# Kernel tuning notes

Measured on AMD Instinct MI355X. Metric: run time of the kernel, lower is better.

The kernel has to match this reference:

```python
import jax, jax.numpy as jnp
import numpy as np


def _l2norm(t, eps=1e-12):
    # matches torch F.normalize(p=2, dim=-1): x / max(||x||_2, eps)
    n = jnp.sqrt(jnp.sum(t * t, axis=-1, keepdims=True))
    return t / jnp.maximum(n, eps)


def setup_inputs() -> dict:
    key = jax.random.key(0)
    ks = jax.random.split(key, 8)
    B, N, C, H, W = 16, 4, 256, 64, 64
    d = 64  # dim_head
    x = jax.random.normal(ks[0], (B, C, H, W), jnp.float32)
    fmaps = jax.random.normal(ks[1], (B, N, C, H, W), jnp.float32)
    Wq = jax.random.normal(ks[2], (N * d, C), jnp.float32) * 0.02   # Linear [out,in]
    Wk = jax.random.normal(ks[3], (N, d, C), jnp.float32) * 0.02    # grouped 1x1 conv, per-group [d,C]
    Wv = jax.random.normal(ks[4], (N, d, C), jnp.float32) * 0.02
    rescale = jnp.ones((N, 1, 1), jnp.float32)
    Wffn = jax.random.normal(ks[5], (C, N * d), jnp.float32) * 0.02
    bffn = jnp.zeros((C,), jnp.float32)
    return {"x": x, "fmaps": fmaps, "Wq": Wq, "Wk": Wk, "Wv": Wv,
            "rescale": rescale, "Wffn": Wffn, "bffn": bffn}


def reference(x, fmaps, Wq, Wk, Wv, rescale, Wffn, bffn):
    B, N, C, H, W = fmaps.shape
    d = Wk.shape[1]
    HW = H * W

    # x: [B,C,H,W] -> tokens [B,HW,C]
    x_in = jnp.transpose(x, (0, 2, 3, 1)).reshape(B, HW, C)
    q_in = jnp.einsum('bsc,oc->bso', x_in, Wq)            # [B,HW,N*d]

    # grouped 1x1 convs on fmaps (group = fmap index n)
    fm = fmaps.reshape(B, N, C, HW)                       # [B,N,C,HW]
    k = jnp.einsum('bncs,ndc->bnds', fm, Wk)              # [B,N,d,HW]
    v = jnp.einsum('bncs,ndc->bnds', fm, Wv)              # [B,N,d,HW]

    q = jnp.transpose(q_in.reshape(B, HW, N, d), (0, 2, 3, 1))  # [B,N,d,HW]

    qn = _l2norm(q)   # normalize over spatial (HW) axis
    kn = _l2norm(k)

    attn = jnp.einsum('bnds,bnes->bnde', kn, qn) * rescale      # [B,N,d,d]
    attn = jax.nn.softmax(attn, axis=-1)
    out = jnp.einsum('bnde,bnes->bnds', attn, v)                # [B,N,d,HW]

    out = jnp.transpose(out, (0, 3, 1, 2)).reshape(B, HW, N * d)  # [B,HW,N*d]
    out = out + q_in
    out = jnp.einsum('bsi,ci->bsc', out, Wffn) + bffn + q_in      # ffn + residual
    return jnp.transpose(out.reshape(B, H, W, C), (0, 3, 1, 2))   # [B,C,H,W]
```

## Files before the change

### kernel.cpp

```cpp
#include <hip/hip_runtime.h>
#include <hip/hip_bf16.h>
#include <cmath>

using bf16 = __hip_bfloat16;
typedef __attribute__((ext_vector_type(4))) float  f32x4;
typedef __attribute__((ext_vector_type(8))) short  bf16x8;
typedef unsigned int u32;
typedef unsigned short u16;

__device__ __forceinline__ void gl_lds16(const bf16* g, bf16* l) {
    __builtin_amdgcn_global_load_lds(
        (const __attribute__((address_space(1))) u32*)g,
        (__attribute__((address_space(3))) u32*)l, 16, 0, 0);
}

__device__ __forceinline__ u32 pk2(float a, float b) {
    bf16 ha = __float2bfloat16(a), hb = __float2bfloat16(b);
    return (u32)*(u16*)&ha | ((u32)*(u16*)&hb << 16);
}

__global__ __launch_bounds__(256) void qproj(
    const float* __restrict__ x,
    const bf16* __restrict__ Wq,
    bf16* __restrict__ qch)
{
    __shared__ bf16 sW[128 * 64];
    __shared__ bf16 sX[128 * 72];
    const int t = threadIdx.x;
    const int lane = t & 63, wid = t >> 6;
    const int wm = wid >> 1, wn = wid & 1;
    const int g = lane >> 4, lr = lane & 15;
    const int s0 = blockIdx.x * 128;
    const int o0 = blockIdx.y * 128;
    const float* xb = x + (long)blockIdx.z * 1048576;

    f32x4 acc[4][4];
#pragma unroll
    for (int i = 0; i < 4; ++i)
#pragma unroll
        for (int j = 0; j < 4; ++j) acc[i][j] = (f32x4){0.f, 0.f, 0.f, 0.f};

    const int p  = t & 31;
    const int sl = t >> 5;

    for (int c0 = 0; c0 < 256; c0 += 64) {
        __syncthreads();
#pragma unroll
        for (int i = 0; i < 4; ++i) {
            int lin = i * 256 + t, r = lin >> 3, ch = lin & 7;
            gl_lds16(Wq + (long)(o0 + r) * 256 + c0 + ((ch ^ (r & 7)) << 3), &sW[lin * 8]);
        }
#pragma unroll
        for (int j = 0; j < 4; ++j) {
            int s4 = j * 8 + sl;
            const float* src = xb + (long)(c0 + 2 * p) * 4096 + s0 + s4 * 4;
            float4 a = *(const float4*)src;
            float4 bq = *(const float4*)(src + 4096);
            char* base = (char*)sX + p * 4 + (s4 * 4) * 144;
            *(u32*)(base +   0) = pk2(a.x, bq.x);
            *(u32*)(base + 144) = pk2(a.y, bq.y);
            *(u32*)(base + 288) = pk2(a.z, bq.z);
            *(u32*)(base + 432) = pk2(a.w, bq.w);
        }
        __syncthreads();
#pragma unroll
        for (int kk = 0; kk < 2; ++kk) {
            bf16x8 aw[4], fx[4];
#pragma unroll
            for (int mf = 0; mf < 4; ++mf) {
                int r = wm * 64 + mf * 16 + lr;
                int ch = (kk * 4 + g) ^ (r & 7);
                aw[mf] = *(const bf16x8*)((const char*)sW + r * 128 + ch * 16);
            }
#pragma unroll
            for (int nf = 0; nf < 4; ++nf) {
                int s = wn * 64 + nf * 16 + lr;
                fx[nf] = *(const bf16x8*)((const char*)sX + s * 144 + (kk * 4 + g) * 16);
            }
#pragma unroll
            for (int mf = 0; mf < 4; ++mf)
#pragma unroll
                for (int nf = 0; nf < 4; ++nf)
                    acc[mf][nf] = __builtin_amdgcn_mfma_f32_16x16x32_bf16(
                        aw[mf], fx[nf], acc[mf][nf], 0, 0, 0);
        }
    }
    bf16* qb = qch + (long)blockIdx.z * 1048576;
#pragma unroll
    for (int mf = 0; mf < 4; ++mf)
#pragma unroll
        for (int nf = 0; nf < 4; ++nf)
#pragma unroll
            for (int e = 0; e < 4; ++e) {
                int o = o0 + wm * 64 + mf * 16 + g * 4 + e;
                int s = s0 + wn * 64 + nf * 16 + lr;
                qb[(long)o * 4096 + s] = __float2bfloat16(acc[mf][nf][e]);
            }
}

__global__ __launch_bounds__(256) void kvproj(
    const float* __restrict__ fm,
    const bf16* __restrict__ Wk,
    const bf16* __restrict__ Wv,
    bf16* __restrict__ kb,
    bf16* __restrict__ vT)
{
    __shared__ bf16 sF[128 * 72];
    __shared__ bf16 sK[64 * 64];
    __shared__ bf16 sV[64 * 64];
    const int t = threadIdx.x;
    const int lane = t & 63, wid = t >> 6;
    const int g = lane >> 4, lr = lane & 15;
    const int s0 = blockIdx.x * 128;
    const int bn = blockIdx.y, n = bn & 3;
    const float* fb = fm + (long)bn * 1048576;
    const bf16* WkN = Wk + (long)n * 16384;
    const bf16* WvN = Wv + (long)n * 16384;

    f32x4 acc1[4][2];
    f32x4 acc2[2][4];
#pragma unroll
    for (int i = 0; i < 4; ++i)
#pragma unroll
        for (int j = 0; j < 2; ++j) {
            acc1[i][j] = (f32x4){0.f, 0.f, 0.f, 0.f};
            acc2[j][i] = (f32x4){0.f, 0.f, 0.f, 0.f};
        }

    const int p  = t & 31;
    const int sl = t >> 5;

    for (int c0 = 0; c0 < 256; c0 += 64) {
        __syncthreads();
#pragma unroll
        for (int i = 0; i < 2; ++i) {
            int lin = i * 256 + t, r = lin >> 3, ch = lin & 7;
            int srcoff = r * 256 + c0 + ((ch ^ (r & 7)) << 3);
            gl_lds16(WkN + srcoff, &sK[lin * 8]);
            gl_lds16(WvN + srcoff, &sV[lin * 8]);
        }
#pragma unroll
        for (int j = 0; j < 4; ++j) {
            int s4 = j * 8 + sl;
            const float* src = fb + (long)(c0 + 2 * p) * 4096 + s0 + s4 * 4;
            float4 a = *(const float4*)src;
            float4 bq = *(const float4*)(src + 4096);
            char* base = (char*)sF + p * 4 + (s4 * 4) * 144;
            *(u32*)(base +   0) = pk2(a.x, bq.x);
            *(u32*)(base + 144) = pk2(a.y, bq.y);
            *(u32*)(base + 288) = pk2(a.z, bq.z);
            *(u32*)(base + 432) = pk2(a.w, bq.w);
        }
        __syncthreads();
#pragma unroll
        for (int kk = 0; kk < 2; ++kk) {
            bf16x8 ak[4], ff[2], bv[4];
#pragma unroll
            for (int mf = 0; mf < 4; ++mf) {
                int r = mf * 16 + lr;
                int ch = (kk * 4 + g) ^ (r & 7);
                ak[mf] = *(const bf16x8*)((const char*)sK + r * 128 + ch * 16);
            }
#pragma unroll
            for (int i = 0; i < 2; ++i) {
                int s = wid * 32 + i * 16 + lr;
                ff[i] = *(const bf16x8*)((const char*)sF + s * 144 + (kk * 4 + g) * 16);
            }
#pragma unroll
            for (int nf = 0; nf < 4; ++nf) {
                int r = nf * 16 + lr;
                int ch = (kk * 4 + g) ^ (r & 7);
                bv[nf] = *(const bf16x8*)((const char*)sV + r * 128 + ch * 16);
            }
#pragma unroll
            for (int mf = 0; mf < 4; ++mf)
#pragma unroll
                for (int i = 0; i < 2; ++i)
                    acc1[mf][i] = __builtin_amdgcn_mfma_f32_16x16x32_bf16(
                        ak[mf], ff[i], acc1[mf][i], 0, 0, 0);
#pragma unroll
            for (int i = 0; i < 2; ++i)
#pragma unroll
                for (int nf = 0; nf < 4; ++nf)
                    acc2[i][nf] = __builtin_amdgcn_mfma_f32_16x16x32_bf16(
                        ff[i], bv[nf], acc2[i][nf], 0, 0, 0);
        }
    }
    bf16* kbb = kb + (long)bn * 262144;
#pragma unroll
    for (int mf = 0; mf < 4; ++mf)
#pragma unroll
        for (int i = 0; i < 2; ++i)
#pragma unroll
            for (int e = 0; e < 4; ++e) {
                int dd = mf * 16 + g * 4 + e;
                int s  = s0 + wid * 32 + i * 16 + lr;
                kbb[(long)dd * 4096 + s] = __float2bfloat16(acc1[mf][i][e]);
            }
    bf16* vtb = vT + (long)bn * 262144;
#pragma unroll
    for (int i = 0; i < 2; ++i)
#pragma unroll
        for (int nf = 0; nf < 4; ++nf)
#pragma unroll
            for (int e = 0; e < 4; ++e) {
                int s = s0 + wid * 32 + i * 16 + g * 4 + e;
                int ec = nf * 16 + lr;
                vtb[(long)s * 64 + ec] = __float2bfloat16(acc2[i][nf][e]);
            }
}

template<int BM, int BN, int EPI>
__global__ __launch_bounds__(256) void gemm_bt(
    const bf16* __restrict__ Ab, const bf16* __restrict__ Bb,
    void* __restrict__ Yb, const bf16* __restrict__ Rb,
    const float* __restrict__ bias,
    int K, int ldA, int ldB, int ldY, int bshift,
    long sAhi, long sAlo, long sBhi, long sBlo, long sYhi, long sYlo)
{
    constexpr int WM = BM / 2, WN = BN / 2;
    constexpr int MF = WM / 16, NF = WN / 16;
    __shared__ bf16 sA[BM * 64];
    __shared__ bf16 sB[BN * 64];

    const int t = threadIdx.x;
    const int lane = t & 63;
    const int wid = t >> 6;
    const int wm = wid >> 1, wn = wid & 1;
    const int g = lane >> 4, lr = lane & 15;

    const int bz = blockIdx.z;
    const long hi = bz >> bshift;
    const long lo = bz & ((1 << bshift) - 1);
    const bf16* A = Ab + hi * sAhi + lo * sAlo + (long)blockIdx.y * BM * ldA;
    const bf16* B = Bb + hi * sBhi + lo * sBlo + (long)blockIdx.x * BN * ldB;

    f32x4 acc[MF][NF];
#pragma unroll
    for (int mf = 0; mf < MF; ++mf)
#pragma unroll
        for (int nf = 0; nf < NF; ++nf) acc[mf][nf] = (f32x4){0.f, 0.f, 0.f, 0.f};

    for (int k0 = 0; k0 < K; k0 += 64) {
        __syncthreads();
#pragma unroll
        for (int i = 0; i < BM / 32; ++i) {
            int lin = i * 256 + t, r = lin >> 3, ch = lin & 7;
            gl_lds16(A + (long)r * ldA + k0 + ((ch ^ (r & 7)) << 3), &sA[lin * 8]);
        }
#pragma unroll
        for (int i = 0; i < BN / 32; ++i) {
            int lin = i * 256 + t, r = lin >> 3, ch = lin & 7;
            gl_lds16(B + (long)r * ldB + k0 + ((ch ^ (r & 7)) << 3), &sB[lin * 8]);
        }
        __syncthreads();
#pragma unroll
        for (int kk = 0; kk < 2; ++kk) {
            bf16x8 af[MF], bfr[NF];
#pragma unroll
            for (int mf = 0; mf < MF; ++mf) {
                int r = wm * WM + mf * 16 + lr;
                int ch = (kk * 4 + g) ^ (r & 7);
                af[mf] = *(const bf16x8*)((const char*)sA + r * 128 + ch * 16);
            }
#pragma unroll
            for (int nf = 0; nf < NF; ++nf) {
                int r = wn * WN + nf * 16 + lr;
                int ch = (kk * 4 + g) ^ (r & 7);
                bfr[nf] = *(const bf16x8*)((const char*)sB + r * 128 + ch * 16);
            }
#pragma unroll
            for (int mf = 0; mf < MF; ++mf)
#pragma unroll
                for (int nf = 0; nf < NF; ++nf)
                    acc[mf][nf] = __builtin_amdgcn_mfma_f32_16x16x32_bf16(
                        af[mf], bfr[nf], acc[mf][nf], 0, 0, 0);
        }
    }

    const long ybase = hi * sYhi + lo * sYlo;
    const int m0 = blockIdx.y * BM + wm * WM;
    const int n0 = blockIdx.x * BN + wn * WN;
#pragma unroll
    for (int mf = 0; mf < MF; ++mf)
#pragma unroll
        for (int nf = 0; nf < NF; ++nf)
#pragma unroll
            for (int e = 0; e < 4; ++e) {
                int m = m0 + mf * 16 + g * 4 + e;
                int n = n0 + nf * 16 + lr;
                long idx = ybase + (long)m * ldY + n;
                float v = acc[mf][nf][e];
                if (EPI == 2) v += __bfloat162float(Rb[idx]) + bias[m];
                ((float*)Yb)[idx] = v;
            }
}

__global__ __launch_bounds__(256) void pv2(
    const bf16* __restrict__ vT,
    const bf16* __restrict__ attnb,
    const bf16* __restrict__ qch,
    bf16* __restrict__ Z)
{
    __shared__ bf16 sVt[128 * 64];
    __shared__ bf16 sAt[64 * 64];
    const int t = threadIdx.x;
    const int lane = t & 63, wid = t >> 6;
    const int wm = wid >> 1, wn = wid & 1;
    const int g = lane >> 4, lr = lane & 15;
    const int s0 = blockIdx.x * 128;
    const int bn = blockIdx.y, b = bn >> 2, n = bn & 3;

#pragma unroll
    for (int i = 0; i < 4; ++i) {
        int lin = i * 256 + t, r = lin >> 3, ch = lin & 7;
        gl_lds16(vT + (long)bn * 262144 + (long)(s0 + r) * 64 + ((ch ^ (r & 7)) << 3),
                 &sVt[lin * 8]);
    }
#pragma unroll
    for (int i = 0; i < 2; ++i) {
        int lin = i * 256 + t, r = lin >> 3, ch = lin & 7;
        gl_lds16(attnb + (long)bn * 4096 + r * 64 + ((ch ^ (r & 7)) << 3), &sAt[lin * 8]);
    }
    __syncthreads();

    f32x4 acc[4][2];
#pragma unroll
    for (int i = 0; i < 4; ++i)
#pragma unroll
        for (int j = 0; j < 2; ++j) acc[i][j] = (f32x4){0.f, 0.f, 0.f, 0.f};

#pragma unroll
    for (int kk = 0; kk < 2; ++kk) {
        bf16x8 av[4], bt[2];
#pragma unroll
        for (int mf = 0; mf < 4; ++mf) {
            int r = wm * 64 + mf * 16 + lr;
            int ch = (kk * 4 + g) ^ (r & 7);
            av[mf] = *(const bf16x8*)((const char*)sVt + r * 128 + ch * 16);
        }
#pragma unroll
        for (int nf = 0; nf < 2; ++nf) {
            int r = wn * 32 + nf * 16 + lr;
            int ch = (kk * 4 + g) ^ (r & 7);
            bt[nf] = *(const bf16x8*)((const char*)sAt + r * 128 + ch * 16);
        }
#pragma unroll
        for (int mf = 0; mf < 4; ++mf)
#pragma unroll
            for (int nf = 0; nf < 2; ++nf)
                acc[mf][nf] = __builtin_amdgcn_mfma_f32_16x16x32_bf16(
                    av[mf], bt[nf], acc[mf][nf], 0, 0, 0);
    }

    bf16* Zb = Z + (long)b * 1048576;
    const bf16* qb = qch + (long)b * 1048576;
#pragma unroll
    for (int mf = 0; mf < 4; ++mf)
#pragma unroll
        for (int nf = 0; nf < 2; ++nf) {
            int c = n * 64 + wn * 32 + nf * 16 + lr;
            int sbase = s0 + wm * 64 + mf * 16 + g * 4;
            ushort4 qv = *(const ushort4*)(qb + (long)c * 4096 + sbase);
            u16 qa[4] = {qv.x, qv.y, qv.z, qv.w};
#pragma unroll
            for (int e = 0; e < 4; ++e) {
                float r2 = __uint_as_float((u32)qa[e] << 16);
                Zb[(long)(sbase + e) * 256 + c] =
                    __float2bfloat16(acc[mf][nf][e] + r2);
            }
        }
}

__global__ __launch_bounds__(256) void wconv(
    const float* __restrict__ a, const float* __restrict__ b,
    const float* __restrict__ c, const float* __restrict__ d,
    bf16* __restrict__ o)
{
    int i = blockIdx.x * 256 + threadIdx.x;
    int which = i >> 16, off = i & 65535;
    const float* s = (which == 0) ? a : (which == 1) ? b : (which == 2) ? c : d;
    o[i] = __float2bfloat16(s[off]);
}

__global__ __launch_bounds__(256) void normk(
    const bf16* __restrict__ qch, const bf16* __restrict__ kb,
    float* __restrict__ invq, float* __restrict__ invk)
{
    int row = blockIdx.x;
    const bf16* base = (row < 4096) ? qch + (long)row * 4096
                                    : kb + (long)(row - 4096) * 4096;
    int t = threadIdx.x;
    float s = 0.f;
#pragma unroll
    for (int h = 0; h < 2; ++h) {
        uint4 v = *(const uint4*)(base + h * 2048 + t * 8);
        u32 ws[4] = {v.x, v.y, v.z, v.w};
#pragma unroll
        for (int j = 0; j < 4; ++j) {
            float lo = __uint_as_float(ws[j] << 16);
            float hi2 = __uint_as_float(ws[j] & 0xffff0000u);
            s += lo * lo + hi2 * hi2;
        }
    }
    __shared__ float red[256];
    red[t] = s;
    __syncthreads();
    for (int off = 128; off > 0; off >>= 1) {
        if (t < off) red[t] += red[t + off];
        __syncthreads();
    }
    if (t == 0) {
        float inv = 1.0f / fmaxf(sqrtf(red[0]), 1e-12f);
        if (row < 4096) invq[row] = inv;
        else            invk[row - 4096] = inv;
    }
}

__global__ __launch_bounds__(256) void attn_finalize_kernel(
    const float* __restrict__ part,
    const float* __restrict__ invq, const float* __restrict__ invk,
    const float* __restrict__ rescale,
    bf16* __restrict__ attn_out)
{
    const int bn = blockIdx.x;
    const int n = bn & 3;
    const int t = threadIdx.x;
    const float rs = rescale[n];

    __shared__ float att[64][65];
    __shared__ float rmax[64], rsum[64];

    const float* pb = part + (size_t)bn * 4 * 4096;
#pragma unroll
    for (int p = 0; p < 16; ++p) {
        int lin = p * 256 + t;
        int dd = lin >> 6, e = lin & 63;
        float v = pb[lin] + pb[4096 + lin] + pb[8192 + lin] + pb[12288 + lin];
        v *= invk[bn * 64 + dd] * invq[bn * 64 + e] * rs;
        att[dd][e] = v;
    }
    __syncthreads();
    if (t < 64) {
        float m = -1e30f;
        for (int e = 0; e < 64; ++e) m = fmaxf(m, att[t][e]);
        float sm = 0.f;
        for (int e = 0; e < 64; ++e) sm += expf(att[t][e] - m);
        rmax[t] = m;
        rsum[t] = 1.0f / sm;
    }
    __syncthreads();
    bf16* ob = attn_out + (size_t)bn * 4096;
#pragma unroll
    for (int p = 0; p < 16; ++p) {
        int lin = p * 256 + t;
        int dd = lin >> 6, e = lin & 63;
        ob[lin] = __float2bfloat16(expf(att[dd][e] - rmax[dd]) * rsum[dd]);
    }
}

extern "C" void kernel_launch(void* const* d_in, const int* in_sizes, int n_in,
                              void* d_out, int out_size, void* d_ws, size_t ws_size,
                              hipStream_t stream) {
    const float* x       = (const float*)d_in[0];
    const float* fmaps   = (const float*)d_in[1];
    const float* Wq      = (const float*)d_in[2];
    const float* Wk      = (const float*)d_in[3];
    const float* Wv      = (const float*)d_in[4];
    const float* rescale = (const float*)d_in[5];
    const float* Wffn    = (const float*)d_in[6];
    const float* bffn    = (const float*)d_in[7];
    float* out = (float*)d_out;

    char* w = (char*)d_ws;
    bf16* kbuf  = (bf16*)(w + 0);
    bf16* Z     = kbuf;
    bf16* vT    = (bf16*)(w + 33554432L);
    bf16* qch   = (bf16*)(w + 67108864L);
    float* part = (float*)(w + 100663296L);
    bf16* attnb = (bf16*)(w + 104857600L);
    float* invq = (float*)(w + 105381888L);
    float* invk = (float*)(w + 105398272L);
    bf16* Wq_b  = (bf16*)(w + 105414656L);
    bf16* Wk_b  = Wq_b + 65536;
    bf16* Wv_b  = Wq_b + 131072;
    bf16* Wf_b  = Wq_b + 196608;

    dim3 blk(256);
    const long BS = 1048576;

    wconv<<<dim3(1024), blk, 0, stream>>>(Wq, Wk, Wv, Wffn, Wq_b);
    kvproj<<<dim3(32, 64), blk, 0, stream>>>(fmaps, Wk_b, Wv_b, kbuf, vT);
    qproj<<<dim3(32, 2, 16), blk, 0, stream>>>(x, Wq_b, qch);
    normk<<<dim3(8192), blk, 0, stream>>>(qch, kbuf, invq, invk);
    gemm_bt<64, 64, 3><<<dim3(1, 1, 256), blk, 0, stream>>>(
        kbuf, qch, part, nullptr, nullptr,
        1024, 4096, 4096, 64, 2,
        262144, 1024, 262144, 1024, 16384, 4096);
    attn_finalize_kernel<<<dim3(64), blk, 0, stream>>>(part, invq, invk, rescale, attnb);
    pv2<<<dim3(32, 64), blk, 0, stream>>>(vT, attnb, qch, Z);
    gemm_bt<128, 128, 2><<<dim3(32, 2, 16), blk, 0, stream>>>(
        Wf_b, Z, out, qch, bffn,
        256, 256, 256, 4096, 0,
        0, 0, BS, 0, BS, 0);
}
```

Before: 201.3 us.

## Fuse norm sums into QK gemm and fuse PV with FFN projection

The separate normk reduction is replaced by a qk_sum kernel that accumulates the squared norms of K and Q rows from the LDS tiles it already loads for the K·Qᵀ partial products, using atomics into a memset buffer. The PV matmul, residual add, and FFN GEMM are fused into one pvffn kernel that keeps the Z tile in LDS and loops over the four heads. This removes the extra read of q/k for the norms and the Z round-trip to global memory. In exchange, pvffn has a large accumulator (32 f32x4 per thread) and only 512 blocks, and qk_sum runs just 256 blocks, so occupancy and parallelism drop.

New measurement: 200.9 us. About the same (-0.2%).

```diff
diff --git a/kernel.cpp b/kernel.cpp
--- a/kernel.cpp
+++ b/kernel.cpp
@@ -17,6 +17,9 @@
 __device__ __forceinline__ u32 pk2(float a, float b) {
     bf16 ha = __float2bfloat16(a), hb = __float2bfloat16(b);
     return (u32)*(u16*)&ha | ((u32)*(u16*)&hb << 16);
+}
+__device__ __forceinline__ float b2f(u16 v) {
+    return __uint_as_float((u32)v << 16);
 }
 
 __global__ __launch_bounds__(256) void qproj(
@@ -210,164 +213,264 @@
             }
 }
 
-template<int BM, int BN, int EPI>
-__global__ __launch_bounds__(256) void gemm_bt(
-    const bf16* __restrict__ Ab, const bf16* __restrict__ Bb,
-    void* __restrict__ Yb, const bf16* __restrict__ Rb,
-    const float* __restrict__ bias,
-    int K, int ldA, int ldB, int ldY, int bshift,
-    long sAhi, long sAlo, long sBhi, long sBlo, long sYhi, long sYlo)
+__global__ __launch_bounds__(256) void qk_sum(
+    const bf16* __restrict__ kb,
+    const bf16* __restrict__ qch,
+    float* __restrict__ part,
+    float* __restrict__ sumq, float* __restrict__ sumk)
 {
-    constexpr int WM = BM / 2, WN = BN / 2;
-    constexpr int MF = WM / 16, NF = WN / 16;
-    __shared__ bf16 sA[BM * 64];
-    __shared__ bf16 sB[BN * 64];
-
-    const int t = threadIdx.x;
-    const int lane = t & 63;
-    const int wid = t >> 6;
-    const int wm = wid >> 1, wn = wid & 1;
-    const int g = lane >> 4, lr = lane & 15;
-
-    const int bz = blockIdx.z;
-    const long hi = bz >> bshift;
-    const long lo = bz & ((1 << bshift) - 1);
-    const bf16* A = Ab + hi * sAhi + lo * sAlo + (long)blockIdx.y * BM * ldA;
-    const bf16* B = Bb + hi * sBhi + lo * sBlo + (long)blockIdx.x * BN * ldB;
-
-    f32x4 acc[MF][NF];
-#pragma unroll
-    for (int mf = 0; mf < MF; ++mf)
-#pragma unroll
-        for (int nf = 0; nf < NF; ++nf) acc[mf][nf] = (f32x4){0.f, 0.f, 0.f, 0.f};
-
-    for (int k0 = 0; k0 < K; k0 += 64) {
-        __syncthreads();
-#pragma unroll
-        for (int i = 0; i < BM / 32; ++i) {
-            int lin = i * 256 + t, r = lin >> 3, ch = lin & 7;
-            gl_lds16(A + (long)r * ldA + k0 + ((ch ^ (r & 7)) << 3), &sA[lin * 8]);
-        }
-#pragma unroll
-        for (int i = 0; i < BN / 32; ++i) {
-            int lin = i * 256 + t, r = lin >> 3, ch = lin & 7;
-            gl_lds16(B + (long)r * ldB + k0 + ((ch ^ (r & 7)) << 3), &sB[lin * 8]);
-        }
-        __syncthreads();
-#pragma unroll
-        for (int kk = 0; kk < 2; ++kk) {
-            bf16x8 af[MF], bfr[NF];
-#pragma unroll
-            for (int mf = 0; mf < MF; ++mf) {
-                int r = wm * WM + mf * 16 + lr;
-                int ch = (kk * 4 + g) ^ (r & 7);
-                af[mf] = *(const bf16x8*)((const char*)sA + r * 128 + ch * 16);
-            }
-#pragma unroll
-            for (int nf = 0; nf < NF; ++nf) {
-                int r = wn * WN + nf * 16 + lr;
-                int ch = (kk * 4 + g) ^ (r & 7);
-                bfr[nf] = *(const bf16x8*)((const char*)sB + r * 128 + ch * 16);
-            }
-#pragma unroll
-            for (int mf = 0; mf < MF; ++mf)
-#pragma unroll
-                for (int nf = 0; nf < NF; ++nf)
-                    acc[mf][nf] = __builtin_amdgcn_mfma_f32_16x16x32_bf16(
-                        af[mf], bfr[nf], acc[mf][nf], 0, 0, 0);
-        }
-    }
-
-    const long ybase = hi * sYhi + lo * sYlo;
-    const int m0 = blockIdx.y * BM + wm * WM;
-    const int n0 = blockIdx.x * BN + wn * WN;
-#pragma unroll
-    for (int mf = 0; mf < MF; ++mf)
-#pragma unroll
-        for (int nf = 0; nf < NF; ++nf)
-#pragma unroll
-            for (int e = 0; e < 4; ++e) {
-                int m = m0 + mf * 16 + g * 4 + e;
-                int n = n0 + nf * 16 + lr;
-                long idx = ybase + (long)m * ldY + n;
-                float v = acc[mf][nf][e];
-                if (EPI == 2) v += __bfloat162float(Rb[idx]) + bias[m];
-                ((float*)Yb)[idx] = v;
-            }
-}
-
-__global__ __launch_bounds__(256) void pv2(
-    const bf16* __restrict__ vT,
-    const bf16* __restrict__ attnb,
-    const bf16* __restrict__ qch,
-    bf16* __restrict__ Z)
-{
-    __shared__ bf16 sVt[128 * 64];
-    __shared__ bf16 sAt[64 * 64];
+    __shared__ bf16 sA[64 * 64];
+    __shared__ bf16 sB[64 * 64];
     const int t = threadIdx.x;
     const int lane = t & 63, wid = t >> 6;
     const int wm = wid >> 1, wn = wid & 1;
     const int g = lane >> 4, lr = lane & 15;
+    const int ch_ = blockIdx.x;
+    const int bn = blockIdx.y;
+    const bf16* kbase = kb + (long)bn * 262144;
+    const bf16* qbase = qch + (long)bn * 262144;
+
+    const int srow = t >> 1;
+    const int shalf = t & 1;
+
+    f32x4 acc[2][2];
+#pragma unroll
+    for (int i = 0; i < 2; ++i)
+#pragma unroll
+        for (int j = 0; j < 2; ++j) acc[i][j] = (f32x4){0.f, 0.f, 0.f, 0.f};
+    float ss = 0.f;
+
+    for (int it = 0; it < 16; ++it) {
+        int k0 = ch_ * 1024 + it * 64;
+        __syncthreads();
+#pragma unroll
+        for (int i = 0; i < 2; ++i) {
+            int lin = i * 256 + t, r = lin >> 3, c = lin & 7;
+            gl_lds16(kbase + (long)r * 4096 + k0 + ((c ^ (r & 7)) << 3), &sA[lin * 8]);
+            gl_lds16(qbase + (long)r * 4096 + k0 + ((c ^ (r & 7)) << 3), &sB[lin * 8]);
+        }
+        __syncthreads();
+#pragma unroll
+        for (int kk = 0; kk < 2; ++kk) {
+            bf16x8 af[2], bf[2];
+#pragma unroll
+            for (int mf = 0; mf < 2; ++mf) {
+                int r = wm * 32 + mf * 16 + lr;
+                af[mf] = *(const bf16x8*)((const char*)sA + r * 128 + (((kk * 4 + g) ^ (r & 7)) << 4));
+            }
+#pragma unroll
+            for (int nf = 0; nf < 2; ++nf) {
+                int r = wn * 32 + nf * 16 + lr;
+                bf[nf] = *(const bf16x8*)((const char*)sB + r * 128 + (((kk * 4 + g) ^ (r & 7)) << 4));
+            }
+#pragma unroll
+            for (int mf = 0; mf < 2; ++mf)
+#pragma unroll
+                for (int nf = 0; nf < 2; ++nf)
+                    acc[mf][nf] = __builtin_amdgcn_mfma_f32_16x16x32_bf16(
+                        af[mf], bf[nf], acc[mf][nf], 0, 0, 0);
+        }
+        {
+            const char* base = (srow < 64) ? (const char*)sA + srow * 128
+                                           : (const char*)sB + (srow - 64) * 128;
+            int r7 = srow & 7;
+#pragma unroll
+            for (int j = 0; j < 4; ++j) {
+                bf16x8 v = *(const bf16x8*)(base + (((shalf * 4 + j) ^ r7) << 4));
+#pragma unroll
+                for (int e = 0; e < 8; ++e) {
+                    float f = b2f((u16)v[e]);
+                    ss += f * f;
+                }
+            }
+        }
+    }
+    ss += __shfl_xor(ss, 1);
+    if (shalf == 0) {
+        if (srow < 64) atomicAdd(&sumk[bn * 64 + srow], ss);
+        else           atomicAdd(&sumq[bn * 64 + srow - 64], ss);
+    }
+    float* pp = part + ((long)bn * 4 + ch_) * 4096;
+#pragma unroll
+    for (int mf = 0; mf < 2; ++mf)
+#pragma unroll
+        for (int nf = 0; nf < 2; ++nf)
+#pragma unroll
+            for (int e = 0; e < 4; ++e) {
+                int m = wm * 32 + mf * 16 + g * 4 + e;
+                int nn = wn * 32 + nf * 16 + lr;
+                pp[m * 64 + nn] = acc[mf][nf][e];
+            }
+}
+
+__global__ __launch_bounds__(256) void attn_finalize_kernel(
+    const float* __restrict__ part,
+    const float* __restrict__ sumq, const float* __restrict__ sumk,
+    const float* __restrict__ rescale,
+    bf16* __restrict__ attn_out)
+{
+    const int bn = blockIdx.x;
+    const int n = bn & 3;
+    const int t = threadIdx.x;
+    const float rs = rescale[n];
+
+    __shared__ float att[64][65];
+    __shared__ float rmax[64], rsum[64];
+    __shared__ float iq[64], ik[64];
+
+    if (t < 64)        ik[t]      = 1.f / fmaxf(sqrtf(sumk[bn * 64 + t]), 1e-12f);
+    else if (t < 128)  iq[t - 64] = 1.f / fmaxf(sqrtf(sumq[bn * 64 + t - 64]), 1e-12f);
+    __syncthreads();
+
+    const float* pb = part + (size_t)bn * 4 * 4096;
+#pragma unroll
+    for (int p = 0; p < 16; ++p) {
+        int lin = p * 256 + t;
+        int dd = lin >> 6, e = lin & 63;
+        float v = pb[lin] + pb[4096 + lin] + pb[8192 + lin] + pb[12288 + lin];
+        v *= ik[dd] * iq[e] * rs;
+        att[dd][e] = v;
+    }
+    __syncthreads();
+    if (t < 64) {
+        float m = -1e30f;
+        for (int e = 0; e < 64; ++e) m = fmaxf(m, att[t][e]);
+        float sm = 0.f;
+        for (int e = 0; e < 64; ++e) sm += expf(att[t][e] - m);
+        rmax[t] = m;
+        rsum[t] = 1.0f / sm;
+    }
+    __syncthreads();
+    bf16* ob = attn_out + (size_t)bn * 4096;
+#pragma unroll
+    for (int p = 0; p < 16; ++p) {
+        int lin = p * 256 + t;
+        int dd = lin >> 6, e = lin & 63;
+        ob[lin] = __float2bfloat16(expf(att[dd][e] - rmax[dd]) * rsum[dd]);
+    }
+}
+
+__global__ __launch_bounds__(256) void pvffn(
+    const bf16* __restrict__ vT,
+    const bf16* __restrict__ attnb,
+    const bf16* __restrict__ qch,
+    const bf16* __restrict__ Wf,
+    const float* __restrict__ bffn,
+    float* __restrict__ out)
+{
+    __shared__ bf16 bufX[256 * 64];
+    __shared__ bf16 Zs[128 * 64];
+    const int t = threadIdx.x;
+    const int lane = t & 63, wid = t >> 6;
+    const int g = lane >> 4, lr = lane & 15;
     const int s0 = blockIdx.x * 128;
-    const int bn = blockIdx.y, b = bn >> 2, n = bn & 3;
-
-#pragma unroll
-    for (int i = 0; i < 4; ++i) {
-        int lin = i * 256 + t, r = lin >> 3, ch = lin & 7;
-        gl_lds16(vT + (long)bn * 262144 + (long)(s0 + r) * 64 + ((ch ^ (r & 7)) << 3),
-                 &sVt[lin * 8]);
-    }
-#pragma unroll
-    for (int i = 0; i < 2; ++i) {
-        int lin = i * 256 + t, r = lin >> 3, ch = lin & 7;
-        gl_lds16(attnb + (long)bn * 4096 + r * 64 + ((ch ^ (r & 7)) << 3), &sAt[lin * 8]);
-    }
-    __syncthreads();
-
-    f32x4 acc[4][2];
+    const int b = blockIdx.y;
+
+    f32x4 accF[4][8];
 #pragma unroll
     for (int i = 0; i < 4; ++i)
 #pragma unroll
-        for (int j = 0; j < 2; ++j) acc[i][j] = (f32x4){0.f, 0.f, 0.f, 0.f};
-
-#pragma unroll
-    for (int kk = 0; kk < 2; ++kk) {
-        bf16x8 av[4], bt[2];
-#pragma unroll
-        for (int mf = 0; mf < 4; ++mf) {
-            int r = wm * 64 + mf * 16 + lr;
-            int ch = (kk * 4 + g) ^ (r & 7);
-            av[mf] = *(const bf16x8*)((const char*)sVt + r * 128 + ch * 16);
-        }
-#pragma unroll
-        for (int nf = 0; nf < 2; ++nf) {
-            int r = wn * 32 + nf * 16 + lr;
-            int ch = (kk * 4 + g) ^ (r & 7);
-            bt[nf] = *(const bf16x8*)((const char*)sAt + r * 128 + ch * 16);
-        }
-#pragma unroll
-        for (int mf = 0; mf < 4; ++mf)
-#pragma unroll
-            for (int nf = 0; nf < 2; ++nf)
-                acc[mf][nf] = __builtin_amdgcn_mfma_f32_16x16x32_bf16(
-                    av[mf], bt[nf], acc[mf][nf], 0, 0, 0);
-    }
-
-    bf16* Zb = Z + (long)b * 1048576;
+        for (int j = 0; j < 8; ++j) accF[i][j] = (f32x4){0.f, 0.f, 0.f, 0.f};
+
+    for (int n = 0; n < 4; ++n) {
+        const int bn = b * 4 + n;
+        __syncthreads();
+#pragma unroll
+        for (int i = 0; i < 4; ++i) {
+            int lin = i * 256 + t, r = lin >> 3, c = lin & 7;
+            gl_lds16(vT + (long)bn * 262144 + (long)(s0 + r) * 64 + ((c ^ (r & 7)) << 3),
+                     &bufX[lin * 8]);
+        }
+#pragma unroll
+        for (int i = 0; i < 2; ++i) {
+            int lin = i * 256 + t, r = lin >> 3, c = lin & 7;
+            gl_lds16(attnb + (long)bn * 4096 + r * 64 + ((c ^ (r & 7)) << 3),
+                     &bufX[8192 + lin * 8]);
+        }
+        __syncthreads();
+        f32x4 accP[2][4];
+#pragma unroll
+        for (int i = 0; i < 2; ++i)
+#pragma unroll
+            for (int j = 0; j < 4; ++j) accP[i][j] = (f32x4){0.f, 0.f, 0.f, 0.f};
+#pragma unroll
+        for (int kk = 0; kk < 2; ++kk) {
+            bf16x8 av[2], at[4];
+#pragma unroll
+            for (int mf = 0; mf < 2; ++mf) {
+                int r = wid * 32 + mf * 16 + lr;
+                av[mf] = *(const bf16x8*)((const char*)bufX + r * 128 + (((kk * 4 + g) ^ (r & 7)) << 4));
+            }
+#pragma unroll
+            for (int nf = 0; nf < 4; ++nf) {
+                int r = nf * 16 + lr;
+                at[nf] = *(const bf16x8*)((const char*)bufX + 16384 + r * 128 + (((kk * 4 + g) ^ (r & 7)) << 4));
+            }
+#pragma unroll
+            for (int mf = 0; mf < 2; ++mf)
+#pragma unroll
+                for (int nf = 0; nf < 4; ++nf)
+                    accP[mf][nf] = __builtin_amdgcn_mfma_f32_16x16x32_bf16(
+                        av[mf], at[nf], accP[mf][nf], 0, 0, 0);
+        }
+#pragma unroll
+        for (int mf = 0; mf < 2; ++mf)
+#pragma unroll
+            for (int nf = 0; nf < 4; ++nf) {
+                int slb = wid * 32 + mf * 16 + g * 4;
+                int il = nf * 16 + lr;
+                ushort4 qv = *(const ushort4*)(qch + ((long)b * 256 + n * 64 + il) * 4096 + s0 + slb);
+                u16 qa[4] = {qv.x, qv.y, qv.z, qv.w};
+#pragma unroll
+                for (int e = 0; e < 4; ++e) {
+                    int sl = slb + e;
+                    float v = accP[mf][nf][e] + b2f(qa[e]);
+                    bf16 hv = __float2bfloat16(v);
+                    int byte = sl * 128 + ((((il >> 3) ^ (sl & 7))) << 4) + (il & 7) * 2;
+                    *(u16*)((char*)Zs + byte) = *(u16*)&hv;
+                }
+            }
+        __syncthreads();
+#pragma unroll
+        for (int i = 0; i < 8; ++i) {
+            int lin = i * 256 + t, r = lin >> 3, c = lin & 7;
+            gl_lds16(Wf + (long)r * 256 + n * 64 + ((c ^ (r & 7)) << 3), &bufX[lin * 8]);
+        }
+        __syncthreads();
+#pragma unroll
+        for (int kk = 0; kk < 2; ++kk) {
+            bf16x8 aw[4], bz[8];
+#pragma unroll
+            for (int mf = 0; mf < 4; ++mf) {
+                int r = wid * 64 + mf * 16 + lr;
+                aw[mf] = *(const bf16x8*)((const char*)bufX + r * 128 + (((kk * 4 + g) ^ (r & 7)) << 4));
+            }
+#pragma unroll
+            for (int nf = 0; nf < 8; ++nf) {
+                int sl = nf * 16 + lr;
+                bz[nf] = *(const bf16x8*)((const char*)Zs + sl * 128 + (((kk * 4 + g) ^ (sl & 7)) << 4));
+            }
+#pragma unroll
+            for (int mf = 0; mf < 4; ++mf)
+#pragma unroll
+                for (int nf = 0; nf < 8; ++nf)
+                    accF[mf][nf] = __builtin_amdgcn_mfma_f32_16x16x32_bf16(
+                        aw[mf], bz[nf], accF[mf][nf], 0, 0, 0);
+        }
+    }
+    float* ob = out + (long)b * 1048576;
     const bf16* qb = qch + (long)b * 1048576;
 #pragma unroll
     for (int mf = 0; mf < 4; ++mf)
 #pragma unroll
-        for (int nf = 0; nf < 2; ++nf) {
-            int c = n * 64 + wn * 32 + nf * 16 + lr;
-            int sbase = s0 + wm * 64 + mf * 16 + g * 4;
-            ushort4 qv = *(const ushort4*)(qb + (long)c * 4096 + sbase);
-            u16 qa[4] = {qv.x, qv.y, qv.z, qv.w};
-#pragma unroll
-            for (int e = 0; e < 4; ++e) {
-                float r2 = __uint_as_float((u32)qa[e] << 16);
-                Zb[(long)(sbase + e) * 256 + c] =
-                    __float2bfloat16(acc[mf][nf][e] + r2);
+        for (int e = 0; e < 4; ++e) {
+            int c = wid * 64 + mf * 16 + g * 4 + e;
+            float bv = bffn[c];
+#pragma unroll
+            for (int nf = 0; nf < 8; ++nf) {
+                int s = s0 + nf * 16 + lr;
+                long idx = (long)c * 4096 + s;
+                ob[idx] = accF[mf][nf][e] + bv + b2f(*(const u16*)(qb + idx));
             }
         }
 }
@@ -381,82 +484,6 @@
     int which = i >> 16, off = i & 65535;
     const float* s = (which == 0) ? a : (which == 1) ? b : (which == 2) ? c : d;
     o[i] = __float2bfloat16(s[off]);
-}
-
-__global__ __launch_bounds__(256) void normk(
-    const bf16* __restrict__ qch, const bf16* __restrict__ kb,
-    float* __restrict__ invq, float* __restrict__ invk)
-{
-    int row = blockIdx.x;
-    const bf16* base = (row < 4096) ? qch + (long)row * 4096
-                                    : kb + (long)(row - 4096) * 4096;
-    int t = threadIdx.x;
-    float s = 0.f;
-#pragma unroll
-    for (int h = 0; h < 2; ++h) {
-        uint4 v = *(const uint4*)(base + h * 2048 + t * 8);
-        u32 ws[4] = {v.x, v.y, v.z, v.w};
-#pragma unroll
-        for (int j = 0; j < 4; ++j) {
-            float lo = __uint_as_float(ws[j] << 16);
-            float hi2 = __uint_as_float(ws[j] & 0xffff0000u);
-            s += lo * lo + hi2 * hi2;
-        }
-    }
-    __shared__ float red[256];
-    red[t] = s;
-    __syncthreads();
-    for (int off = 128; off > 0; off >>= 1) {
-        if (t < off) red[t] += red[t + off];
-        __syncthreads();
-    }
-    if (t == 0) {
-        float inv = 1.0f / fmaxf(sqrtf(red[0]), 1e-12f);
-        if (row < 4096) invq[row] = inv;
-        else            invk[row - 4096] = inv;
-    }
-}
-
-__global__ __launch_bounds__(256) void attn_finalize_kernel(
-    const float* __restrict__ part,
-    const float* __restrict__ invq, const float* __restrict__ invk,
-    const float* __restrict__ rescale,
-    bf16* __restrict__ attn_out)
-{
-    const int bn = blockIdx.x;
-    const int n = bn & 3;
-    const int t = threadIdx.x;
-    const float rs = rescale[n];
-
-    __shared__ float att[64][65];
-    __shared__ float rmax[64], rsum[64];
-
-    const float* pb = part + (size_t)bn * 4 * 4096;
-#pragma unroll
-    for (int p = 0; p < 16; ++p) {
-        int lin = p * 256 + t;
-        int dd = lin >> 6, e = lin & 63;
-        float v = pb[lin] + pb[4096 + lin] + pb[8192 + lin] + pb[12288 + lin];
-        v *= invk[bn * 64 + dd] * invq[bn * 64 + e] * rs;
-        att[dd][e] = v;
-    }
-    __syncthreads();
-    if (t < 64) {
-        float m = -1e30f;
-        for (int e = 0; e < 64; ++e) m = fmaxf(m, att[t][e]);
-        float sm = 0.f;
-        for (int e = 0; e < 64; ++e) sm += expf(att[t][e] - m);
-        rmax[t] = m;
-        rsum[t] = 1.0f / sm;
-    }
-    __syncthreads();
-    bf16* ob = attn_out + (size_t)bn * 4096;
-#pragma unroll
-    for (int p = 0; p < 16; ++p) {
-        int lin = p * 256 + t;
-        int dd = lin >> 6, e = lin & 63;
-        ob[lin] = __float2bfloat16(expf(att[dd][e] - rmax[dd]) * rsum[dd]);
-    }
 }
 
 extern "C" void kernel_launch(void* const* d_in, const int* in_sizes, int n_in,
@@ -474,33 +501,24 @@
 
     char* w = (char*)d_ws;
     bf16* kbuf  = (bf16*)(w + 0);
-    bf16* Z     = kbuf;
     bf16* vT    = (bf16*)(w + 33554432L);
     bf16* qch   = (bf16*)(w + 67108864L);
     float* part = (float*)(w + 100663296L);
     bf16* attnb = (bf16*)(w + 104857600L);
-    float* invq = (float*)(w + 105381888L);
-    float* invk = (float*)(w + 105398272L);
+    float* sumq = (float*)(w + 105381888L);
+    float* sumk = (float*)(w + 105398272L);
     bf16* Wq_b  = (bf16*)(w + 105414656L);
     bf16* Wk_b  = Wq_b + 65536;
     bf16* Wv_b  = Wq_b + 131072;
     bf16* Wf_b  = Wq_b + 196608;
 
     dim3 blk(256);
-    const long BS = 1048576;
-
+
+    hipMemsetAsync(sumq, 0, 32768, stream);
     wconv<<<dim3(1024), blk, 0, stream>>>(Wq, Wk, Wv, Wffn, Wq_b);
     kvproj<<<dim3(32, 64), blk, 0, stream>>>(fmaps, Wk_b, Wv_b, kbuf, vT);
     qproj<<<dim3(32, 2, 16), blk, 0, stream>>>(x, Wq_b, qch);
-    normk<<<dim3(8192), blk, 0, stream>>>(qch, kbuf, invq, invk);
-    gemm_bt<64, 64, 3><<<dim3(1, 1, 256), blk, 0, stream>>>(
-        kbuf, qch, part, nullptr, nullptr,
-        1024, 4096, 4096, 64, 2,
-        262144, 1024, 262144, 1024, 16384, 4096);
-    attn_finalize_kernel<<<dim3(64), blk, 0, stream>>>(part, invq, invk, rescale, attnb);
-    pv2<<<dim3(32, 64), blk, 0, stream>>>(vT, attnb, qch, Z);
-    gemm_bt<128, 128, 2><<<dim3(32, 2, 16), blk, 0, stream>>>(
-        Wf_b, Z, out, qch, bffn,
-        256, 256, 256, 4096, 0,
-        0, 0, BS, 0, BS, 0);
-}
+    qk_sum<<<dim3(4, 64), blk, 0, stream>>>(kbuf, qch, part, sumq, sumk);
+    attn_finalize_kernel<<<dim3(64), blk, 0, stream>>>(part, sumq, sumk, rescale, attnb);
+    pvffn<<<dim3(32, 16), blk, 0, stream>>>(vT, attnb, qch, Wf_b, bffn, out);
+}
```
